# Performance work log

Measured on AMD Instinct MI355X. Metric: run time of the kernel, lower is better.

## Reference

```python
import jax, jax.numpy as jnp
import numpy as np

R_SPHERE = 1.0   # conf['object_bounding_sphere']
N_STEPS = 64     # conf['n_steps']
N_IMPORT = 32    # forward default num_samples
VARI = 0.3       # forward default vari -> inv_s = exp(3)


def sdf_fn(pts):
    # analytic stand-in for implicit_network(x, expression)[..., 0]: sphere of radius 0.5
    return jnp.linalg.norm(pts, axis=-1) - 0.5


def sample_pdf(bins, weights, n_samples):
    # deterministic (det=True) CDF inversion, faithful to sample_pdf()
    weights = weights + 1e-8
    pdf = weights / jnp.sum(weights, -1, keepdims=True)
    cdf = jnp.cumsum(pdf, -1)
    cdf = jnp.concatenate([jnp.zeros_like(cdf[..., :1]), cdf], -1)  # [R, n]
    u = jnp.linspace(0.5 / n_samples, 1.0 - 0.5 / n_samples, n_samples, dtype=bins.dtype)
    u = jnp.broadcast_to(u, cdf.shape[:-1] + (n_samples,))          # [R, ns]
    inds = jax.vmap(lambda c, uu: jnp.searchsorted(c, uu, side='right'))(cdf, u)
    below = jnp.maximum(inds - 1, 0)
    above = jnp.minimum(inds, cdf.shape[-1] - 1)
    cdf_b = jnp.take_along_axis(cdf, below, -1)
    cdf_a = jnp.take_along_axis(cdf, above, -1)
    bins_b = jnp.take_along_axis(bins, below, -1)
    bins_a = jnp.take_along_axis(bins, above, -1)
    denom = cdf_a - cdf_b
    denom = jnp.where(denom < 1e-8, jnp.ones_like(denom), denom)
    t = (u - cdf_b) / denom
    return bins_b + t * (bins_a - bins_b)


def setup_inputs() -> dict:
    key = jax.random.key(0)
    k1, k2 = jax.random.split(key)
    rd = jax.random.normal(k1, (1, 262144, 3), dtype=jnp.float32)
    rd = rd / jnp.linalg.norm(rd, axis=-1, keepdims=True)  # unit ray directions
    cam_loc = jnp.array([[0.0, 0.0, 2.5]], dtype=jnp.float32)  # outside bounding sphere
    t_rand = jax.random.uniform(k2, (262144, N_STEPS), dtype=jnp.float32)
    return {"ray_dirs": rd, "cam_loc": cam_loc, "t_rand": t_rand}


def reference(ray_dirs, cam_loc, t_rand):
    b, p, _ = ray_dirs.shape
    # --- get_sphere_intersection ---
    ray_cam_dot = jnp.einsum('bpd,bd->bp', ray_dirs, cam_loc)              # [b,p]
    under = ray_cam_dot ** 2 - (jnp.sum(cam_loc ** 2, -1, keepdims=True) - R_SPHERE ** 2)
    under = under.reshape(-1)
    mask = under > 0
    sq = jnp.sqrt(jnp.where(mask, under, 0.0))
    si = sq[:, None] * jnp.array([-1.0, 1.0], dtype=ray_dirs.dtype) - ray_cam_dot.reshape(-1)[:, None]
    n_hit = jnp.maximum(jnp.sum(mask), 1)
    mean_si = jnp.sum(jnp.where(mask[:, None], si, 0.0), 0) / n_hit
    si = jnp.where(mask[:, None], si, mean_si[None, :])
    si = jnp.clip(si, 0.0, None)                                           # [b*p, 2]
    min_d, max_d = si[:, 0], si[:, 1]
    # --- eval_sdf_inside_sphere: stratified uniform samples (mask_intersect == all ones) ---
    steps = jnp.linspace(0.0, 1.0, N_STEPS, dtype=ray_dirs.dtype)[None, :]
    steps = steps * (max_d - min_d)[:, None] + min_d[:, None]
    sample_dist = ((max_d - min_d) / N_STEPS)[:, None]
    steps = steps + (t_rand - 0.5) * sample_dist                           # [R, n]
    origins = jnp.broadcast_to(cam_loc[:, None, :], (b, p, 3)).reshape(-1, 3)
    dirs = ray_dirs.reshape(-1, 3)
    pts = origins[:, None, :] + steps[..., None] * dirs[:, None, :]        # [R, n, 3]
    sdf = sdf_fn(pts)                                                      # [R, n]
    # --- NeuS alpha / weights ---
    inv_s = jnp.exp(jnp.asarray(VARI, ray_dirs.dtype) * 10.0)
    prev_cdf = jax.nn.sigmoid(sdf[:, :-1] * inv_s)
    next_cdf = jax.nn.sigmoid(sdf[:, 1:] * inv_s)
    alpha = jnp.clip((prev_cdf - next_cdf + 1e-8) / (prev_cdf + 1e-8), 0.0, 1.0)
    trans = jnp.cumprod(jnp.concatenate([jnp.ones((alpha.shape[0], 1), alpha.dtype),
                                         1.0 - alpha + 1e-7], -1), -1)[:, :-1]
    weights = alpha * trans                                                # [R, n-1]
    # --- up_sample: PDF importance resampling (searchsorted + gather) ---
    z_samples = sample_pdf(steps, weights, N_IMPORT)                       # [R, ns]
    new_samples = origins[:, None, :] + z_samples[..., None] * dirs[:, None, :]  # [R, ns, 3]
    return new_samples, z_samples, weights
```

## Files before the change

### kernel.cpp

```cpp
#include <hip/hip_runtime.h>


static constexpr int NSTEPS = 64;
static constexpr int NIMP   = 32;

__global__ __launch_bounds__(256) void si_partial_kernel(
    const float* __restrict__ rd, const float* __restrict__ cam,
    float* __restrict__ partial, int P)
{
  float cx = cam[0], cy = cam[1], cz = cam[2];
  float c2m = cx*cx + cy*cy + cz*cz - 1.0f;
  float s0 = 0.f, s1 = 0.f, cnt = 0.f;
  int stride = gridDim.x * blockDim.x;
  for (int p = blockIdx.x * blockDim.x + threadIdx.x; p < P; p += stride){
    float dx = rd[3*p+0], dy = rd[3*p+1], dz = rd[3*p+2];
    float rcd = dx*cx + dy*cy + dz*cz;
    float under = rcd*rcd - c2m;
    if (under > 0.f){
      float sq = sqrtf(under);
      s0 += -sq - rcd; s1 += sq - rcd; cnt += 1.f;
    }
  }
  #pragma unroll
  for (int off = 32; off > 0; off >>= 1){
    s0  += __shfl_down(s0,  off, 64);
    s1  += __shfl_down(s1,  off, 64);
    cnt += __shfl_down(cnt, off, 64);
  }
  __shared__ float sh[3][4];
  int w = threadIdx.x >> 6;
  if ((threadIdx.x & 63) == 0){ sh[0][w] = s0; sh[1][w] = s1; sh[2][w] = cnt; }
  __syncthreads();
  if (threadIdx.x == 0){
    partial[blockIdx.x*3+0] = sh[0][0]+sh[0][1]+sh[0][2]+sh[0][3];
    partial[blockIdx.x*3+1] = sh[1][0]+sh[1][1]+sh[1][2]+sh[1][3];
    partial[blockIdx.x*3+2] = sh[2][0]+sh[2][1]+sh[2][2]+sh[2][3];
  }
}

__global__ __launch_bounds__(256) void si_final_kernel(
    const float* __restrict__ partial, float* __restrict__ ws, int nblk)
{
  float s0 = 0.f, s1 = 0.f, cnt = 0.f;
  for (int b = threadIdx.x; b < nblk; b += 256){
    s0 += partial[3*b+0]; s1 += partial[3*b+1]; cnt += partial[3*b+2];
  }
  #pragma unroll
  for (int off = 32; off > 0; off >>= 1){
    s0  += __shfl_down(s0,  off, 64);
    s1  += __shfl_down(s1,  off, 64);
    cnt += __shfl_down(cnt, off, 64);
  }
  __shared__ float sh[3][4];
  int w = threadIdx.x >> 6;
  if ((threadIdx.x & 63) == 0){ sh[0][w] = s0; sh[1][w] = s1; sh[2][w] = cnt; }
  __syncthreads();
  if (threadIdx.x == 0){
    ws[0] = sh[0][0]+sh[0][1]+sh[0][2]+sh[0][3];
    ws[1] = sh[1][0]+sh[1][1]+sh[1][2]+sh[1][3];
    ws[2] = sh[2][0]+sh[2][1]+sh[2][2]+sh[2][3];
  }
}

__global__ __launch_bounds__(256, 4) void render_main_kernel(
    const float* __restrict__ rd, const float* __restrict__ cam,
    const float* __restrict__ tr, const float* __restrict__ ws,
    float* __restrict__ out, int P)
{
  __shared__ float lds[9472];
  const int tid  = threadIdx.x;
  const int blk  = blockIdx.x;
  const int ray0 = blk * 256;
  const int nrays = min(256, P - ray0);
  const int p = min(ray0 + tid, P - 1);

  float cx = cam[0], cy = cam[1], cz = cam[2];
  float c2m = cx*cx + cy*cy + cz*cz - 1.0f;
  float dx = rd[3*p+0], dy = rd[3*p+1], dz = rd[3*p+2];
  lds[8448 + tid*4 + 0] = dx;
  lds[8448 + tid*4 + 1] = dy;
  lds[8448 + tid*4 + 2] = dz;

  float rcd = dx*cx + dy*cy + dz*cz;
  float under = rcd*rcd - c2m;
  float si0, si1;
  if (under > 0.f){
    float sq = sqrtf(under);
    si0 = -sq - rcd; si1 = sq - rcd;
  } else {
    float nh = fmaxf(ws[2], 1.0f);
    si0 = ws[0] / nh; si1 = ws[1] / nh;
  }
  float min_d = fmaxf(si0, 0.f), max_d = fmaxf(si1, 0.f);
  float range = max_d - min_d;
  float sdist = range * (1.0f / NSTEPS);

  const float4* tr4 = (const float4*)(tr + (size_t)p * NSTEPS);
  const float inv_s = 20.085536923187668f;

  float w[NSTEPS-1];
  float T = 0.f, trans = 1.f;
  float4 v = tr4[0];
  float st = min_d + (v.x - 0.5f) * sdist;
  float px = fmaf(st,dx,cx), py = fmaf(st,dy,cy), pz = fmaf(st,dz,cz);
  float c0 = 1.0f / (1.0f + __expf(-(sqrtf(px*px+py*py+pz*pz) - 0.5f) * inv_s));
  #pragma unroll
  for (int j = 1; j < NSTEPS; j++){
    if ((j & 3) == 0) v = tr4[j >> 2];
    float tj = ((j&3)==0) ? v.x : ((j&3)==1) ? v.y : ((j&3)==2) ? v.z : v.w;
    float sn = fmaf(range, (float)j * (1.0f/63.0f), min_d) + (tj - 0.5f) * sdist;
    float qx = fmaf(sn,dx,cx), qy = fmaf(sn,dy,cy), qz = fmaf(sn,dz,cz);
    float c1 = 1.0f / (1.0f + __expf(-(sqrtf(qx*qx+qy*qy+qz*qz) - 0.5f) * inv_s));
    float a = (c0 - c1 + 1e-8f) / (c0 + 1e-8f);
    a = fminf(fmaxf(a, 0.f), 1.0f);
    float wj = a * trans;
    w[j-1] = wj; T += wj;
    trans *= (1.0f - a + 1e-7f);
    c0 = c1;
  }
  T += 63.0f * 1e-8f;
  float invT = 1.0f / T;

  if (tid < 128){
    #pragma unroll
    for (int j = 0; j < 63; j++) lds[tid*63 + j] = w[j];
  }
  __syncthreads();
  {
    int cnt0 = min(128, nrays);
    if (cnt0 > 0){
      size_t base = (size_t)P*128 + (size_t)ray0*63;
      if (cnt0 == 128){
        float4* gw = (float4*)(out + base);
        const float4* lw = (const float4*)lds;
        #pragma unroll
        for (int it = 0; it < 8; it++){
          int idx = it*256 + tid;
          if (idx < 2016) gw[idx] = lw[idx];
        }
      } else {
        int dwn = cnt0 * 63;
        for (int idx = tid; idx < dwn; idx += 256) out[base + idx] = lds[idx];
      }
    }
  }
  __syncthreads();
  if (tid >= 128){
    #pragma unroll
    for (int j = 0; j < 63; j++) lds[(tid-128)*63 + j] = w[j];
  }
  __syncthreads();
  {
    int cnt1 = nrays - 128;
    if (cnt1 > 0){
      size_t base = (size_t)P*128 + ((size_t)ray0 + 128)*63;
      if (cnt1 == 128){
        float4* gw = (float4*)(out + base);
        const float4* lw = (const float4*)lds;
        #pragma unroll
        for (int it = 0; it < 8; it++){
          int idx = it*256 + tid;
          if (idx < 2016) gw[idx] = lw[idx];
        }
      } else {
        int dwn = cnt1 * 63;
        for (int idx = tid; idx < dwn; idx += 256) out[base + idx] = lds[idx];
      }
    }
  }
  __syncthreads();

  {
    float4 v2 = tr4[0];
    float sm = min_d + (v2.x - 0.5f) * sdist;
    float cdfm = 0.f;
    int i = 0;
    #pragma unroll
    for (int m = 0; m < NSTEPS-1; m++){
      int j = m + 1;
      if ((j & 3) == 0) v2 = tr4[j >> 2];
      float tj = ((j&3)==0) ? v2.x : ((j&3)==1) ? v2.y : ((j&3)==2) ? v2.z : v2.w;
      float sn = fmaf(range, (float)j * (1.0f/63.0f), min_d) + (tj - 0.5f) * sdist;
      float cdfn = cdfm + (w[m] + 1e-8f) * invT;
      while (i < NIMP){
        float u = (float)(2*i + 1) * (1.0f / 64.0f);
        if (!(u < cdfn)) break;
        float denom = cdfn - cdfm;
        if (denom < 1e-8f) denom = 1.0f;
        float t = (u - cdfm) / denom;
        lds[tid*33 + i] = fmaf(t, sn - sm, sm);
        i++;
      }
      cdfm = cdfn; sm = sn;
    }
    while (i < NIMP){ lds[tid*33 + i] = sm; i++; }
  }
  __syncthreads();

  {
    int nz4 = nrays * 8;
    float4* gz = (float4*)(out + (size_t)P*96 + (size_t)ray0*32);
    #pragma unroll
    for (int it = 0; it < 8; it++){
      int idx = it*256 + tid;
      if (idx < nz4){
        int r  = idx >> 3;
        int s0 = (idx & 7) * 4;
        float4 o;
        o.x = lds[r*33 + s0 + 0];
        o.y = lds[r*33 + s0 + 1];
        o.z = lds[r*33 + s0 + 2];
        o.w = lds[r*33 + s0 + 3];
        gz[idx] = o;
      }
    }
  }

  {
    int nn4 = nrays * 24;
    float4* gn = (float4*)(out + (size_t)ray0*96);
    #pragma unroll 4
    for (int it = 0; it < 24; it++){
      int idx4 = it*256 + tid;
      if (idx4 < nn4){
        int r   = idx4 / 24;
        int rem = idx4 - r*24;
        int e   = rem * 4;
        int s   = e / 3;
        int c   = e - s*3;
        float4 o;
        float* op = &o.x;
        #pragma unroll
        for (int k = 0; k < 4; k++){
          float zz = lds[r*33 + s];
          float dd = lds[8448 + r*4 + c];
          float cc = (c == 0) ? cx : ((c == 1) ? cy : cz);
          op[k] = fmaf(zz, dd, cc);
          if (++c == 3){ c = 0; s++; }
        }
        gn[idx4] = o;
      }
    }
  }
}

extern "C" void kernel_launch(void* const* d_in, const int* in_sizes, int n_in,
                              void* d_out, int out_size, void* d_ws, size_t ws_size,
                              hipStream_t stream) {
  const float* rd  = (const float*)d_in[0];
  const float* cam = (const float*)d_in[1];
  const float* tr  = (const float*)d_in[2];
  float* out = (float*)d_out;
  float* ws  = (float*)d_ws;
  const int P = in_sizes[0] / 3;

  const int RBLK = 256;
  si_partial_kernel<<<RBLK, 256, 0, stream>>>(rd, cam, ws + 8, P);
  si_final_kernel<<<1, 256, 0, stream>>>(ws + 8, ws, RBLK);
  render_main_kernel<<<(P + 255) / 256, 256, 0, stream>>>(rd, cam, tr, ws, out, P);
}
```

Before: 320.2 us.

## Map one ray per wavefront with shuffle scans and parallel CDF search

Replaces the one-thread-per-ray kernel with a grid-stride kernel where each 64-lane wavefront handles one ray, one sample per lane. The transmittance cumprod and the CDF become wave-level shuffle scans, and the PDF inversion becomes a per-lane binary search over shuffled CDF values. Outputs are written directly with coalesced per-lane stores, which removes the LDS staging, the per-thread 63-float register array and the block barriers. The cost is many shuffles per ray, and the grid is fixed at 2048 blocks.

New measurement: 310.1 us. 1.03x faster.

```diff
diff --git a/kernel.cpp b/kernel.cpp
--- a/kernel.cpp
+++ b/kernel.cpp
@@ -62,184 +62,102 @@
   }
 }
 
-__global__ __launch_bounds__(256, 4) void render_main_kernel(
+__global__ __launch_bounds__(256) void render_wave_kernel(
     const float* __restrict__ rd, const float* __restrict__ cam,
     const float* __restrict__ tr, const float* __restrict__ ws,
     float* __restrict__ out, int P)
 {
-  __shared__ float lds[9472];
-  const int tid  = threadIdx.x;
-  const int blk  = blockIdx.x;
-  const int ray0 = blk * 256;
-  const int nrays = min(256, P - ray0);
-  const int p = min(ray0 + tid, P - 1);
+  const int lane = threadIdx.x & 63;
+  const int wid  = (int)((blockIdx.x * blockDim.x + threadIdx.x) >> 6);
+  const int nw   = (int)((gridDim.x * blockDim.x) >> 6);
 
-  float cx = cam[0], cy = cam[1], cz = cam[2];
-  float c2m = cx*cx + cy*cy + cz*cz - 1.0f;
-  float dx = rd[3*p+0], dy = rd[3*p+1], dz = rd[3*p+2];
-  lds[8448 + tid*4 + 0] = dx;
-  lds[8448 + tid*4 + 1] = dy;
-  lds[8448 + tid*4 + 2] = dz;
+  const float cx = cam[0], cy = cam[1], cz = cam[2];
+  const float c2m = cx*cx + cy*cy + cz*cz - 1.0f;
+  const float nh = fmaxf(ws[2], 1.0f);
+  const float m0 = ws[0] / nh, m1 = ws[1] / nh;
 
-  float rcd = dx*cx + dy*cy + dz*cz;
-  float under = rcd*rcd - c2m;
-  float si0, si1;
-  if (under > 0.f){
-    float sq = sqrtf(under);
-    si0 = -sq - rcd; si1 = sq - rcd;
-  } else {
-    float nh = fmaxf(ws[2], 1.0f);
-    si0 = ws[0] / nh; si1 = ws[1] / nh;
-  }
-  float min_d = fmaxf(si0, 0.f), max_d = fmaxf(si1, 0.f);
-  float range = max_d - min_d;
-  float sdist = range * (1.0f / NSTEPS);
+  const float inv_s = 20.085536923187668f;
+  const float jf = (float)lane * (1.0f/63.0f);
+  const float u  = (float)(2*lane + 1) * (1.0f/64.0f);
 
-  const float4* tr4 = (const float4*)(tr + (size_t)p * NSTEPS);
-  const float inv_s = 20.085536923187668f;
+  const int e2 = 64 + lane;
+  const int q1 = lane / 3, r1 = lane - 3*q1;
+  const int q2 = e2  / 3, r2 = e2  - 3*q2;
 
-  float w[NSTEPS-1];
-  float T = 0.f, trans = 1.f;
-  float4 v = tr4[0];
-  float st = min_d + (v.x - 0.5f) * sdist;
-  float px = fmaf(st,dx,cx), py = fmaf(st,dy,cy), pz = fmaf(st,dz,cz);
-  float c0 = 1.0f / (1.0f + __expf(-(sqrtf(px*px+py*py+pz*pz) - 0.5f) * inv_s));
-  #pragma unroll
-  for (int j = 1; j < NSTEPS; j++){
-    if ((j & 3) == 0) v = tr4[j >> 2];
-    float tj = ((j&3)==0) ? v.x : ((j&3)==1) ? v.y : ((j&3)==2) ? v.z : v.w;
-    float sn = fmaf(range, (float)j * (1.0f/63.0f), min_d) + (tj - 0.5f) * sdist;
-    float qx = fmaf(sn,dx,cx), qy = fmaf(sn,dy,cy), qz = fmaf(sn,dz,cz);
-    float c1 = 1.0f / (1.0f + __expf(-(sqrtf(qx*qx+qy*qy+qz*qz) - 0.5f) * inv_s));
-    float a = (c0 - c1 + 1e-8f) / (c0 + 1e-8f);
+  for (int p = wid; p < P; p += nw){
+    float dx = rd[3*p+0], dy = rd[3*p+1], dz = rd[3*p+2];
+    float rcd = dx*cx + dy*cy + dz*cz;
+    float under = rcd*rcd - c2m;
+    float si0, si1;
+    if (under > 0.f){
+      float sq = sqrtf(under);
+      si0 = -sq - rcd; si1 = sq - rcd;
+    } else {
+      si0 = m0; si1 = m1;
+    }
+    float min_d = fmaxf(si0, 0.f), max_d = fmaxf(si1, 0.f);
+    float range = max_d - min_d;
+    float sdist = range * (1.0f/64.0f);
+
+    float t = tr[(size_t)p*64 + lane];
+    float s = fmaf(range, jf, min_d) + (t - 0.5f) * sdist;
+    float px = fmaf(s,dx,cx), py = fmaf(s,dy,cy), pz = fmaf(s,dz,cz);
+    float c  = 1.0f / (1.0f + __expf(-(sqrtf(px*px+py*py+pz*pz) - 0.5f) * inv_s));
+
+    float cnx = __shfl_down(c, 1, 64);
+    float a = (c - cnx + 1e-8f) / (c + 1e-8f);
     a = fminf(fmaxf(a, 0.f), 1.0f);
-    float wj = a * trans;
-    w[j-1] = wj; T += wj;
-    trans *= (1.0f - a + 1e-7f);
-    c0 = c1;
-  }
-  T += 63.0f * 1e-8f;
-  float invT = 1.0f / T;
 
-  if (tid < 128){
+    float f = (lane < 63) ? (1.0f - a + 1e-7f) : 1.0f;
+    float incl = f;
     #pragma unroll
-    for (int j = 0; j < 63; j++) lds[tid*63 + j] = w[j];
-  }
-  __syncthreads();
-  {
-    int cnt0 = min(128, nrays);
-    if (cnt0 > 0){
-      size_t base = (size_t)P*128 + (size_t)ray0*63;
-      if (cnt0 == 128){
-        float4* gw = (float4*)(out + base);
-        const float4* lw = (const float4*)lds;
-        #pragma unroll
-        for (int it = 0; it < 8; it++){
-          int idx = it*256 + tid;
-          if (idx < 2016) gw[idx] = lw[idx];
-        }
-      } else {
-        int dwn = cnt0 * 63;
-        for (int idx = tid; idx < dwn; idx += 256) out[base + idx] = lds[idx];
-      }
+    for (int r = 1; r < 64; r <<= 1){
+      float v = __shfl_up(incl, r, 64);
+      if (lane >= r) incl *= v;
     }
-  }
-  __syncthreads();
-  if (tid >= 128){
+    float trans = __shfl_up(incl, 1, 64);
+    if (lane == 0) trans = 1.0f;
+
+    float w = a * trans;
+    if (lane < 63) out[(size_t)P*128 + (size_t)p*63 + lane] = w;
+
+    float wp = (lane < 63) ? (w + 1e-8f) : 0.0f;
+    float D = wp;
     #pragma unroll
-    for (int j = 0; j < 63; j++) lds[(tid-128)*63 + j] = w[j];
-  }
-  __syncthreads();
-  {
-    int cnt1 = nrays - 128;
-    if (cnt1 > 0){
-      size_t base = (size_t)P*128 + ((size_t)ray0 + 128)*63;
-      if (cnt1 == 128){
-        float4* gw = (float4*)(out + base);
-        const float4* lw = (const float4*)lds;
-        #pragma unroll
-        for (int it = 0; it < 8; it++){
-          int idx = it*256 + tid;
-          if (idx < 2016) gw[idx] = lw[idx];
-        }
-      } else {
-        int dwn = cnt1 * 63;
-        for (int idx = tid; idx < dwn; idx += 256) out[base + idx] = lds[idx];
-      }
+    for (int r = 1; r < 64; r <<= 1){
+      float v = __shfl_up(D, r, 64);
+      if (lane >= r) D += v;
     }
-  }
-  __syncthreads();
+    float Tp = __shfl(D, 62, 64);
+    float invT = 1.0f / Tp;
+    D *= invT;
+    if (lane == 63) D = 2.0f;
 
-  {
-    float4 v2 = tr4[0];
-    float sm = min_d + (v2.x - 0.5f) * sdist;
-    float cdfm = 0.f;
-    int i = 0;
+    int js = 0;
     #pragma unroll
-    for (int m = 0; m < NSTEPS-1; m++){
-      int j = m + 1;
-      if ((j & 3) == 0) v2 = tr4[j >> 2];
-      float tj = ((j&3)==0) ? v2.x : ((j&3)==1) ? v2.y : ((j&3)==2) ? v2.z : v2.w;
-      float sn = fmaf(range, (float)j * (1.0f/63.0f), min_d) + (tj - 0.5f) * sdist;
-      float cdfn = cdfm + (w[m] + 1e-8f) * invT;
-      while (i < NIMP){
-        float u = (float)(2*i + 1) * (1.0f / 64.0f);
-        if (!(u < cdfn)) break;
-        float denom = cdfn - cdfm;
-        if (denom < 1e-8f) denom = 1.0f;
-        float t = (u - cdfm) / denom;
-        lds[tid*33 + i] = fmaf(t, sn - sm, sm);
-        i++;
-      }
-      cdfm = cdfn; sm = sn;
+    for (int r = 32; r >= 1; r >>= 1){
+      float v = __shfl(D, js + r - 1, 64);
+      if (v <= u) js += r;
     }
-    while (i < NIMP){ lds[tid*33 + i] = sm; i++; }
-  }
-  __syncthreads();
+    float Db = (js > 0) ? __shfl(D, js - 1, 64) : 0.0f;
+    float Da = __shfl(D, js, 64);
+    float sb = __shfl(s, js, 64);
+    float sa = __shfl(s, js + 1, 64);
+    float den = Da - Db;
+    if (den < 1e-8f) den = 1.0f;
+    float tq = (u - Db) / den;
+    float z  = fmaf(tq, sa - sb, sb);
+    if (lane < 32) out[(size_t)P*96 + (size_t)p*32 + lane] = z;
 
-  {
-    int nz4 = nrays * 8;
-    float4* gz = (float4*)(out + (size_t)P*96 + (size_t)ray0*32);
-    #pragma unroll
-    for (int it = 0; it < 8; it++){
-      int idx = it*256 + tid;
-      if (idx < nz4){
-        int r  = idx >> 3;
-        int s0 = (idx & 7) * 4;
-        float4 o;
-        o.x = lds[r*33 + s0 + 0];
-        o.y = lds[r*33 + s0 + 1];
-        o.z = lds[r*33 + s0 + 2];
-        o.w = lds[r*33 + s0 + 3];
-        gz[idx] = o;
-      }
-    }
-  }
-
-  {
-    int nn4 = nrays * 24;
-    float4* gn = (float4*)(out + (size_t)ray0*96);
-    #pragma unroll 4
-    for (int it = 0; it < 24; it++){
-      int idx4 = it*256 + tid;
-      if (idx4 < nn4){
-        int r   = idx4 / 24;
-        int rem = idx4 - r*24;
-        int e   = rem * 4;
-        int s   = e / 3;
-        int c   = e - s*3;
-        float4 o;
-        float* op = &o.x;
-        #pragma unroll
-        for (int k = 0; k < 4; k++){
-          float zz = lds[r*33 + s];
-          float dd = lds[8448 + r*4 + c];
-          float cc = (c == 0) ? cx : ((c == 1) ? cy : cz);
-          op[k] = fmaf(zz, dd, cc);
-          if (++c == 3){ c = 0; s++; }
-        }
-        gn[idx4] = o;
-      }
+    float z1 = __shfl(z, q1, 64);
+    float dd1 = (r1 == 0) ? dx : ((r1 == 1) ? dy : dz);
+    float cc1 = (r1 == 0) ? cx : ((r1 == 1) ? cy : cz);
+    out[(size_t)p*96 + lane] = fmaf(z1, dd1, cc1);
+    if (lane < 32){
+      float z2 = __shfl(z, q2, 64);
+      float dd2 = (r2 == 0) ? dx : ((r2 == 1) ? dy : dz);
+      float cc2 = (r2 == 0) ? cx : ((r2 == 1) ? cy : cz);
+      out[(size_t)p*96 + e2] = fmaf(z2, dd2, cc2);
     }
   }
 }
@@ -257,5 +175,5 @@
   const int RBLK = 256;
   si_partial_kernel<<<RBLK, 256, 0, stream>>>(rd, cam, ws + 8, P);
   si_final_kernel<<<1, 256, 0, stream>>>(ws + 8, ws, RBLK);
-  render_main_kernel<<<(P + 255) / 256, 256, 0, stream>>>(rd, cam, tr, ws, out, P);
+  render_wave_kernel<<<2048, 256, 0, stream>>>(rd, cam, tr, ws, out, P);
 }
```
